# Kernel optimization log

Measured on AMD Instinct MI355X. Metric: run time of the kernel, lower is better.

The kernel has to match this reference:

```python
import jax, jax.numpy as jnp
import numpy as np

RCR = 5.2
RCA = 3.5
ETA_R = 16.0
ETA_A = 8.0
ZETA = 32.0
NUM_SPECIES = 4
NUM_PAIRS = NUM_SPECIES * (NUM_SPECIES + 1) // 2  # 10
SHFR = jnp.asarray(np.linspace(0.9, RCR, 17)[:-1], dtype=jnp.float32)   # (16,)
SHFA = jnp.asarray(np.linspace(0.9, RCA, 5)[:-1], dtype=jnp.float32)    # (4,)
SHFZ = jnp.asarray((np.linspace(0.0, np.pi, 9) + np.pi / 16.0)[:-1], dtype=jnp.float32)  # (8,)

def _triu_index(n):
    s1, s2 = np.triu_indices(n)
    t = np.zeros((n, n), dtype=np.int32)
    t[s1, s2] = np.arange(len(s1))
    t[s2, s1] = np.arange(len(s1))
    return jnp.asarray(t)

TRIU = _triu_index(NUM_SPECIES)  # (4,4) -> pair index in [0,10)

def _fc(d, rc):
    # cosine cutoff, zero beyond rc
    return jnp.where(d < rc, 0.5 * jnp.cos(np.float32(np.pi) * d / rc) + 0.5, 0.0)

def _aev(species, coordinates):
    N, A = species.shape
    # vec[n,i,j] = r_j - r_i  (N,A,A,3)
    vec = coordinates[:, None, :, :] - coordinates[:, :, None, :]
    d2 = jnp.sum(vec * vec, axis=-1)                      # (N,A,A)
    eye = jnp.eye(A, dtype=bool)
    d = jnp.sqrt(jnp.where(eye, 1.0, d2))                 # safe sqrt on diagonal
    pair_mask = (~eye).astype(coordinates.dtype)          # (A,A)

    # ---- radial AEV ----
    fcr = _fc(d, RCR) * pair_mask                         # (N,A,A)
    rad = 0.25 * jnp.exp(-ETA_R * (d[..., None] - SHFR) ** 2) * fcr[..., None]  # (N,A,A,16)
    sp_oh = jax.nn.one_hot(species, NUM_SPECIES, dtype=coordinates.dtype)       # (N,A,4)
    radial_aev = jnp.einsum('nijt,njs->nist', rad, sp_oh).reshape(N, A, -1)     # (N,A,64)

    # ---- angular AEV ----
    fca = _fc(d, RCA) * pair_mask                         # (N,A,A)
    dot = jnp.einsum('nijc,nikc->nijk', vec, vec)         # (N,A,A,A)
    cosang = 0.95 * dot / jnp.clip(d[:, :, :, None] * d[:, :, None, :], 1e-10)
    angles = jnp.arccos(cosang)                           # (N,A,A,A)
    mask_jk = (~eye).astype(coordinates.dtype)            # j != k
    fcj12 = fca[:, :, :, None] * fca[:, :, None, :] * mask_jk[None, None]  # (N,A,A,A)
    dmean = 0.5 * (d[:, :, :, None] + d[:, :, None, :])   # (N,A,A,A)
    factor1 = ((1.0 + jnp.cos(angles[..., None] - SHFZ)) * 0.5) ** ZETA    # (N,A,A,A,8)
    factor2 = jnp.exp(-ETA_A * (dmean[..., None] - SHFA) ** 2)             # (N,A,A,A,4)
    # terms over ordered (j,k); each unordered pair counted twice, so the
    # original factor 2 and the 0.5 double-count correction cancel.
    terms = (fcj12[..., None] * factor2)[..., :, None] * factor1[..., None, :]  # (N,A,A,A,4,8)
    terms = terms.reshape(N, A, A, A, SHFA.shape[0] * SHFZ.shape[0])            # (N,A,A,A,32)
    pair_idx = TRIU[species[:, :, None], species[:, None, :]]                   # (N,A,A)
    pair_oh = jax.nn.one_hot(pair_idx, NUM_PAIRS, dtype=coordinates.dtype)      # (N,A,A,10)
    angular_aev = jnp.einsum('nijkt,njkp->nipt', terms, pair_oh).reshape(N, A, -1)  # (N,A,320)

    return jnp.concatenate([radial_aev, angular_aev], axis=-1)  # (N,A,384)

def setup_inputs() -> dict:
    key = jax.random.key(0)
    k1, k2 = jax.random.split(key)
    species = jax.random.randint(k1, (32, 48), 0, NUM_SPECIES)
    # atoms in an 8 Angstrom box -> realistic neighbor density for 5.2 A cutoff
    coordinates = jax.random.uniform(k2, (32, 48, 3), dtype=jnp.float32) * 8.0
    return {"species": species, "coordinates": coordinates}

def reference(species, coordinates):
    return _aev(species, coordinates)
```

## Files before the change

kernel.cpp:

```cpp
#include <hip/hip_runtime.h>
#include <math.h>


#define A_ATOMS 48
#define NMOL    32
#define NFEAT   384
#define CHUNK   256

__device__ __constant__ float CZ_TAB[8] = {
     0.980785280f,  0.831469612f,  0.555570233f,  0.195090322f,
    -0.195090322f, -0.555570233f, -0.831469612f, -0.980785280f };
__device__ __constant__ float SZ_TAB[8] = {
     0.195090322f,  0.555570233f,  0.831469612f,  0.980785280f,
     0.980785280f,  0.831469612f,  0.555570233f,  0.195090322f };

__device__ __forceinline__ float bf2f(unsigned short h) {
    return __uint_as_float(((unsigned int)h) << 16);
}

__global__ __launch_bounds__(256, 6)
void AEVComputer_2156073583107_kernel(const void* __restrict__ coords_raw,
                                      const void* __restrict__ species_raw,
                                      float* __restrict__ out)
{
    const int bid   = blockIdx.x;
    const int n     = bid / A_ATOMS;
    const int i     = bid - n * A_ATOMS;
    const int tid   = threadIdx.x;
    const int w     = tid >> 6;
    const int lane  = tid & 63;
    const int sub   = lane >> 5;
    const int slice = (w << 1) | sub;
    const int t     = lane & 31;
    const int ia    = t >> 3;

    __shared__ float dL[A_ATOMS], fcaL[A_ATOMS];
    __shared__ float ux[A_ATOMS], uy[A_ATOMS], uz[A_ATOMS];
    __shared__ int   sp[A_ATOMS], nbr[A_ATOMS];
    __shared__ int   Msh;
    __shared__ float2 pairA[CHUNK];
    __shared__ float  pairW[CHUNK * 4];
    __shared__ int   cnt[10], curs[10], ofs[11];
    __shared__ float rad_m[4][64];
    __shared__ float ang_m[8][320];

    const unsigned short* cu16 = (const unsigned short*)coords_raw;
    const unsigned int*   su32 = (const unsigned int*)species_raw;

    if (tid < 64) {
        float v = bf2f(cu16[tid]);
        unsigned long long mb = __ballot(fabsf(v) < 32.0f);
        const bool coords_bf16 = (__popcll(mb) >= 60);
        unsigned int svv = su32[tid & 31];
        unsigned long long m2 = __ballot((tid < 32) && svv >= 0x3F000000u && svv < 0x40800000u);
        unsigned long long m3 = __ballot((tid < 32) && (tid & 1) && svv != 0u);
        const int smode = (__popcll(m2) > 20) ? 2 : ((m3 == 0ull) ? 1 : 0);

        float x = 0.f, y = 0.f, z = 0.f; int s = 0;
        if (tid < A_ATOMS) {
            const int g = n * A_ATOMS + tid;
            if (coords_bf16) {
                x = bf2f(cu16[3 * g]); y = bf2f(cu16[3 * g + 1]); z = bf2f(cu16[3 * g + 2]);
            } else {
                const float* cf = (const float*)coords_raw;
                x = cf[3 * g]; y = cf[3 * g + 1]; z = cf[3 * g + 2];
            }
            if (smode == 0)      s = ((const int*)species_raw)[g];
            else if (smode == 1) s = ((const int*)species_raw)[2 * g];
            else                 s = (int)(((const float*)species_raw)[g] + 0.5f);
            s = (s < 0) ? 0 : ((s > 3) ? 3 : s);
        }
        const float xi = __shfl(x, i), yi = __shfl(y, i), zi = __shfl(z, i);
        float dx = x - xi, dy = y - yi, dz = z - zi;
        float d2 = dx * dx + dy * dy + dz * dz;
        float d  = (tid == i) ? 1.0f : sqrtf(d2);
        float inv = 1.0f / d;
        bool pred = (tid < A_ATOMS) && (tid != i) && (d < 3.5f);
        float fca = pred ? (0.5f * __cosf(0.8975979010f * d) + 0.5f) : 0.0f;
        if (tid < A_ATOMS) {
            dL[tid] = d;
            ux[tid] = dx * inv; uy[tid] = dy * inv; uz[tid] = dz * inv;
            fcaL[tid] = fca; sp[tid] = s;
        }
        unsigned long long mask = __ballot(pred);
        if (pred) {
            int pos = __popcll(mask & ((1ull << tid) - 1ull));
            nbr[pos] = tid;
        }
        if (tid == 0) Msh = __popcll(mask);
    }
    __syncthreads();
    const int M = Msh;
    const int npairs = (M * (M - 1)) >> 1;

    {
        const int   s    = lane >> 4;
        const int   rt   = lane & 15;
        const float shfr = 0.9f + 0.26875f * (float)rt;
        float radv = 0.0f;
        #pragma unroll
        for (int jj = 0; jj < 12; ++jj) {
            const int j = w + 4 * jj;
            float d   = dL[j];
            float fcr = 0.5f * __cosf(0.6041524333f * d) + 0.5f;
            float e   = d - shfr;
            float val = 0.25f * __expf(-16.0f * e * e) * fcr;
            bool  ok  = (j != i) && (d < 5.2f) && (sp[j] == s);
            radv += ok ? val : 0.0f;
        }
        rad_m[w][lane] = radv;
    }

    float a[10];
    #pragma unroll
    for (int p = 0; p < 10; ++p) a[p] = 0.0f;
    const float czv = CZ_TAB[t & 7];
    const float szv = SZ_TAB[t & 7];

    for (int base = 0; base < npairs; base += CHUNK) {
        if (tid < 10) cnt[tid] = 0;
        __syncthreads();

        const int  q     = base + tid;
        const bool havep = (q < npairs);
        float2 pa; float wf[4]; int p = 0;
        if (havep) {
            const float b = (float)(2 * M - 1);
            int jj = (int)(0.5f * (b - sqrtf(fmaxf(b * b - 8.0f * (float)q, 0.0f))));
            jj = max(0, min(jj, M - 2));
            while (jj > 0 && q < ((jj * (2 * M - 1 - jj)) >> 1)) --jj;
            while (q >= (((jj + 1) * (2 * M - 2 - jj)) >> 1)) ++jj;
            const int kk = jj + 1 + (q - ((jj * (2 * M - 1 - jj)) >> 1));
            const int j = nbr[jj], k = nbr[kk];
            float c  = fmaf(ux[j], ux[k], fmaf(uy[j], uy[k], uz[j] * uz[k]));
            float cc = 0.95f * c;
            float ss = sqrtf(fmaxf(1.0f - cc * cc, 0.0f));
            pa.x = 0.5f * cc;
            pa.y = 0.5f * ss;
            const float wgt = 2.0f * fcaL[j] * fcaL[k];
            const float dm  = 0.5f * (dL[j] + dL[k]);
            #pragma unroll
            for (int q4 = 0; q4 < 4; ++q4) {
                float e = dm - (0.9f + 0.65f * (float)q4);
                wf[q4] = wgt * __expf(-8.0f * e * e);
            }
            const int sj = sp[j], sk = sp[k];
            const int lo = min(sj, sk), hi = max(sj, sk);
            p = ((lo * (7 - lo)) >> 1) + hi;
            atomicAdd(&cnt[p], 1);
        }
        __syncthreads();
        if (tid == 0) {
            int o = 0;
            #pragma unroll
            for (int pp = 0; pp < 10; ++pp) { ofs[pp] = o; curs[pp] = o; o += cnt[pp]; }
            ofs[10] = o;
        }
        __syncthreads();
        if (havep) {
            int slot = atomicAdd(&curs[p], 1);
            pairA[slot] = pa;
            pairW[4 * slot + 0] = wf[0];
            pairW[4 * slot + 1] = wf[1];
            pairW[4 * slot + 2] = wf[2];
            pairW[4 * slot + 3] = wf[3];
        }
        __syncthreads();

        #pragma unroll
        for (int pp = 0; pp < 10; ++pp) {
            const int e1 = ofs[pp + 1];
            float acc = a[pp];
            for (int qq = ofs[pp] + slice; qq < e1; qq += 8) {
                float2 v  = pairA[qq];
                float wf2 = pairW[4 * qq + ia];
                float x   = fmaf(v.y, szv, fmaf(v.x, czv, 0.5f));
                float x2 = x * x, x4 = x2 * x2, x8 = x4 * x4, x16 = x8 * x8;
                acc = fmaf(x16 * x16, wf2, acc);
            }
            a[pp] = acc;
        }
        __syncthreads();
    }

    #pragma unroll
    for (int pp = 0; pp < 10; ++pp) ang_m[slice][pp * 32 + t] = a[pp];
    __syncthreads();

    const size_t outb = (size_t)bid * NFEAT;
    for (int f = tid; f < NFEAT; f += 256) {
        float v;
        if (f < 64) {
            v = rad_m[0][f] + rad_m[1][f] + rad_m[2][f] + rad_m[3][f];
        } else {
            const int g = f - 64;
            v = ((ang_m[0][g] + ang_m[1][g]) + (ang_m[2][g] + ang_m[3][g]))
              + ((ang_m[4][g] + ang_m[5][g]) + (ang_m[6][g] + ang_m[7][g]));
        }
        out[outb + f] = v;
    }
}

extern "C" void kernel_launch(void* const* d_in, const int* in_sizes, int n_in,
                              void* d_out, int out_size, void* d_ws, size_t ws_size,
                              hipStream_t stream) {
    if (n_in < 2) return;
    const void* coords;
    const void* species;
    if (in_sizes[0] >= in_sizes[1]) { coords = d_in[0]; species = d_in[1]; }
    else                            { coords = d_in[1]; species = d_in[0]; }
    float* out = (float*)d_out;
    AEVComputer_2156073583107_kernel<<<NMOL * A_ATOMS, 256, 0, stream>>>(coords, species, out);
}
```

Baseline: 63.93 us.

## Enlarge pair chunk, pack atom geometry into float4, precompute radial cutoff

Raises the pair chunk from 256 to 384 so each thread builds up to two pairs per pass, which cuts the number of chunk iterations and block-wide barriers. Per-atom data (distance, radial cutoff weight, angular cutoff, species, unit vector) is packed into float4 shared arrays so the radial and pair loops use fewer LDS loads, and the radial cutoff cosine is computed once per atom instead of once per thread. Coordinate and species loads are issued early, the first counter reset and the final barrier are skipped, and the angular accumulation loop is unrolled by two. In exchange it uses more shared memory and registers, which may lower occupancy.

New measurement: 61.63 us. 3.6% less time.

```diff
diff --git a/kernel.cpp b/kernel.cpp
--- a/kernel.cpp
+++ b/kernel.cpp
@@ -5,7 +5,7 @@
 #define A_ATOMS 48
 #define NMOL    32
 #define NFEAT   384
-#define CHUNK   256
+#define CHUNK   384
 
 __device__ __constant__ float CZ_TAB[8] = {
      0.980785280f,  0.831469612f,  0.555570233f,  0.195090322f,
@@ -34,20 +34,28 @@
     const int t     = lane & 31;
     const int ia    = t >> 3;
 
-    __shared__ float dL[A_ATOMS], fcaL[A_ATOMS];
-    __shared__ float ux[A_ATOMS], uy[A_ATOMS], uz[A_ATOMS];
-    __shared__ int   sp[A_ATOMS], nbr[A_ATOMS];
-    __shared__ int   Msh;
+    __shared__ float4 geom[A_ATOMS];
+    __shared__ float4 uvec[A_ATOMS];
+    __shared__ int    nbr[A_ATOMS];
+    __shared__ int    Msh;
     __shared__ float2 pairA[CHUNK];
     __shared__ float  pairW[CHUNK * 4];
-    __shared__ int   cnt[10], curs[10], ofs[11];
-    __shared__ float rad_m[4][64];
-    __shared__ float ang_m[8][320];
+    __shared__ int    cnt[10], curs[10], ofs[11];
+    __shared__ float  rad_m[4][64];
+    __shared__ float  ang_m[8][320];
 
     const unsigned short* cu16 = (const unsigned short*)coords_raw;
     const unsigned int*   su32 = (const unsigned int*)species_raw;
 
     if (tid < 64) {
+        if (tid < 10) cnt[tid] = 0;
+        float xf = 0.f, yf = 0.f, zf = 0.f; unsigned int uraw = 0u;
+        if (tid < A_ATOMS) {
+            const int g = n * A_ATOMS + tid;
+            const float* cf = (const float*)coords_raw;
+            xf = cf[3 * g]; yf = cf[3 * g + 1]; zf = cf[3 * g + 2];
+            uraw = su32[g];
+        }
         float v = bf2f(cu16[tid]);
         unsigned long long mb = __ballot(fabsf(v) < 32.0f);
         const bool coords_bf16 = (__popcll(mb) >= 60);
@@ -56,18 +64,14 @@
         unsigned long long m3 = __ballot((tid < 32) && (tid & 1) && svv != 0u);
         const int smode = (__popcll(m2) > 20) ? 2 : ((m3 == 0ull) ? 1 : 0);
 
-        float x = 0.f, y = 0.f, z = 0.f; int s = 0;
+        float x = xf, y = yf, z = zf; int s = 0;
         if (tid < A_ATOMS) {
             const int g = n * A_ATOMS + tid;
             if (coords_bf16) {
                 x = bf2f(cu16[3 * g]); y = bf2f(cu16[3 * g + 1]); z = bf2f(cu16[3 * g + 2]);
-            } else {
-                const float* cf = (const float*)coords_raw;
-                x = cf[3 * g]; y = cf[3 * g + 1]; z = cf[3 * g + 2];
-            }
-            if (smode == 0)      s = ((const int*)species_raw)[g];
-            else if (smode == 1) s = ((const int*)species_raw)[2 * g];
-            else                 s = (int)(((const float*)species_raw)[g] + 0.5f);
+            }
+            if (smode == 1) uraw = su32[2 * g];
+            s = (smode == 2) ? (int)(__uint_as_float(uraw) + 0.5f) : (int)uraw;
             s = (s < 0) ? 0 : ((s > 3) ? 3 : s);
         }
         const float xi = __shfl(x, i), yi = __shfl(y, i), zi = __shfl(z, i);
@@ -75,15 +79,18 @@
         float d2 = dx * dx + dy * dy + dz * dz;
         float d  = (tid == i) ? 1.0f : sqrtf(d2);
         float inv = 1.0f / d;
-        bool pred = (tid < A_ATOMS) && (tid != i) && (d < 3.5f);
-        float fca = pred ? (0.5f * __cosf(0.8975979010f * d) + 0.5f) : 0.0f;
+        bool  self = (tid >= A_ATOMS) || (tid == i);
+        bool  predA = !self && (d < 3.5f);
+        bool  predR = !self && (d < 5.2f);
+        float fca = predA ? (0.5f * __cosf(0.8975979010f * d) + 0.5f) : 0.0f;
+        float rv  = predR ? (0.25f * (0.5f * __cosf(0.6041524333f * d) + 0.5f)) : 0.0f;
         if (tid < A_ATOMS) {
-            dL[tid] = d;
-            ux[tid] = dx * inv; uy[tid] = dy * inv; uz[tid] = dz * inv;
-            fcaL[tid] = fca; sp[tid] = s;
-        }
-        unsigned long long mask = __ballot(pred);
-        if (pred) {
+            float spf = (float)s;
+            geom[tid] = make_float4(d, rv, fca, spf);
+            uvec[tid] = make_float4(dx * inv, dy * inv, dz * inv, spf);
+        }
+        unsigned long long mask = __ballot(predA);
+        if (predA) {
             int pos = __popcll(mask & ((1ull << tid) - 1ull));
             nbr[pos] = tid;
         }
@@ -94,19 +101,15 @@
     const int npairs = (M * (M - 1)) >> 1;
 
     {
-        const int   s    = lane >> 4;
-        const int   rt   = lane & 15;
-        const float shfr = 0.9f + 0.26875f * (float)rt;
+        const float sf   = (float)(lane >> 4);
+        const float shfr = 0.9f + 0.26875f * (float)(lane & 15);
         float radv = 0.0f;
         #pragma unroll
         for (int jj = 0; jj < 12; ++jj) {
-            const int j = w + 4 * jj;
-            float d   = dL[j];
-            float fcr = 0.5f * __cosf(0.6041524333f * d) + 0.5f;
-            float e   = d - shfr;
-            float val = 0.25f * __expf(-16.0f * e * e) * fcr;
-            bool  ok  = (j != i) && (d < 5.2f) && (sp[j] == s);
-            radv += ok ? val : 0.0f;
+            const float4 gm = geom[w + 4 * jj];
+            float e   = gm.x - shfr;
+            float val = __expf(-16.0f * e * e) * gm.y;
+            radv += (gm.w == sf) ? val : 0.0f;
         }
         rad_m[w][lane] = radv;
     }
@@ -118,13 +121,20 @@
     const float szv = SZ_TAB[t & 7];
 
     for (int base = 0; base < npairs; base += CHUNK) {
-        if (tid < 10) cnt[tid] = 0;
-        __syncthreads();
-
-        const int  q     = base + tid;
-        const bool havep = (q < npairs);
-        float2 pa; float wf[4]; int p = 0;
-        if (havep) {
+        if (base > 0) {
+            if (tid < 10) cnt[tid] = 0;
+            __syncthreads();
+        }
+        const int nch = min(CHUNK, npairs - base);
+
+        float2 pa0, pa1; float wf0[4], wf1[4]; int p0 = 0, p1 = 0;
+        const bool h0 = (tid < nch);
+        const bool h1 = (tid + 256 < nch);
+        #pragma unroll
+        for (int pass = 0; pass < 2; ++pass) {
+            const bool hv = pass ? h1 : h0;
+            if (!hv) continue;
+            const int q = base + tid + (pass ? 256 : 0);
             const float b = (float)(2 * M - 1);
             int jj = (int)(0.5f * (b - sqrtf(fmaxf(b * b - 8.0f * (float)q, 0.0f))));
             jj = max(0, min(jj, M - 2));
@@ -132,22 +142,26 @@
             while (q >= (((jj + 1) * (2 * M - 2 - jj)) >> 1)) ++jj;
             const int kk = jj + 1 + (q - ((jj * (2 * M - 1 - jj)) >> 1));
             const int j = nbr[jj], k = nbr[kk];
-            float c  = fmaf(ux[j], ux[k], fmaf(uy[j], uy[k], uz[j] * uz[k]));
+            const float4 gj = geom[j], gk = geom[k];
+            const float4 uj = uvec[j], uk = uvec[k];
+            float c  = fmaf(uj.x, uk.x, fmaf(uj.y, uk.y, uj.z * uk.z));
             float cc = 0.95f * c;
             float ss = sqrtf(fmaxf(1.0f - cc * cc, 0.0f));
-            pa.x = 0.5f * cc;
-            pa.y = 0.5f * ss;
-            const float wgt = 2.0f * fcaL[j] * fcaL[k];
-            const float dm  = 0.5f * (dL[j] + dL[k]);
+            float2 pa = make_float2(0.5f * cc, 0.5f * ss);
+            const float wgt = 2.0f * gj.z * gk.z;
+            const float dm  = 0.5f * (gj.x + gk.x);
+            float wf[4];
             #pragma unroll
             for (int q4 = 0; q4 < 4; ++q4) {
                 float e = dm - (0.9f + 0.65f * (float)q4);
                 wf[q4] = wgt * __expf(-8.0f * e * e);
             }
-            const int sj = sp[j], sk = sp[k];
+            const int sj = (int)gj.w, sk = (int)gk.w;
             const int lo = min(sj, sk), hi = max(sj, sk);
-            p = ((lo * (7 - lo)) >> 1) + hi;
+            const int p = ((lo * (7 - lo)) >> 1) + hi;
             atomicAdd(&cnt[p], 1);
+            if (pass) { pa1 = pa; wf1[0]=wf[0]; wf1[1]=wf[1]; wf1[2]=wf[2]; wf1[3]=wf[3]; p1 = p; }
+            else      { pa0 = pa; wf0[0]=wf[0]; wf0[1]=wf[1]; wf0[2]=wf[2]; wf0[3]=wf[3]; p0 = p; }
         }
         __syncthreads();
         if (tid == 0) {
@@ -157,30 +171,53 @@
             ofs[10] = o;
         }
         __syncthreads();
-        if (havep) {
-            int slot = atomicAdd(&curs[p], 1);
-            pairA[slot] = pa;
-            pairW[4 * slot + 0] = wf[0];
-            pairW[4 * slot + 1] = wf[1];
-            pairW[4 * slot + 2] = wf[2];
-            pairW[4 * slot + 3] = wf[3];
+        if (h0) {
+            int slot = atomicAdd(&curs[p0], 1);
+            pairA[slot] = pa0;
+            pairW[4*slot+0]=wf0[0]; pairW[4*slot+1]=wf0[1];
+            pairW[4*slot+2]=wf0[2]; pairW[4*slot+3]=wf0[3];
+        }
+        if (h1) {
+            int slot = atomicAdd(&curs[p1], 1);
+            pairA[slot] = pa1;
+            pairW[4*slot+0]=wf1[0]; pairW[4*slot+1]=wf1[1];
+            pairW[4*slot+2]=wf1[2]; pairW[4*slot+3]=wf1[3];
         }
         __syncthreads();
 
+        int O[11];
+        #pragma unroll
+        for (int pp = 0; pp < 11; ++pp) O[pp] = ofs[pp];
+
         #pragma unroll
         for (int pp = 0; pp < 10; ++pp) {
-            const int e1 = ofs[pp + 1];
+            const int e1 = O[pp + 1];
+            int qq = O[pp] + slice;
             float acc = a[pp];
-            for (int qq = ofs[pp] + slice; qq < e1; qq += 8) {
-                float2 v  = pairA[qq];
-                float wf2 = pairW[4 * qq + ia];
-                float x   = fmaf(v.y, szv, fmaf(v.x, czv, 0.5f));
-                float x2 = x * x, x4 = x2 * x2, x8 = x4 * x4, x16 = x8 * x8;
-                acc = fmaf(x16 * x16, wf2, acc);
+            for (; qq + 8 < e1; qq += 16) {
+                float2 v0  = pairA[qq];
+                float  w0  = pairW[4 * qq + ia];
+                float2 v1  = pairA[qq + 8];
+                float  w1  = pairW[4 * (qq + 8) + ia];
+                float x0 = fmaf(v0.y, szv, fmaf(v0.x, czv, 0.5f));
+                float x1 = fmaf(v1.y, szv, fmaf(v1.x, czv, 0.5f));
+                float a2 = x0*x0, b2 = x1*x1;
+                float a4 = a2*a2, b4 = b2*b2;
+                float a8 = a4*a4, b8 = b4*b4;
+                float a16 = a8*a8, b16 = b8*b8;
+                acc = fmaf(a16 * a16, w0, acc);
+                acc = fmaf(b16 * b16, w1, acc);
+            }
+            if (qq < e1) {
+                float2 v0 = pairA[qq];
+                float  w0 = pairW[4 * qq + ia];
+                float x0 = fmaf(v0.y, szv, fmaf(v0.x, czv, 0.5f));
+                float a2 = x0*x0, a4 = a2*a2, a8 = a4*a4, a16 = a8*a8;
+                acc = fmaf(a16 * a16, w0, acc);
             }
             a[pp] = acc;
         }
-        __syncthreads();
+        if (base + CHUNK < npairs) __syncthreads();
     }
 
     #pragma unroll
```
